# Optimization experiments

Measured on AMD Instinct MI355X. Metric: run time of the kernel, lower is better.

The kernel has to match this reference:

```python
import jax, jax.numpy as jnp
import numpy as np

PAD_IDX = 0
NEG_INF = -1e30

N_USERS, N_ITEMS, N_SUBJECTS, EMB_DIM = 100000, 100000, 10000, 16
B, L = 16384, 50


def setup_inputs() -> dict:
    key = jax.random.key(0)
    ks = jax.random.split(key, 10)
    subj_emb = jax.random.normal(ks[0], (N_SUBJECTS, EMB_DIM), dtype=jnp.float32) * 0.1
    subj_emb = subj_emb.at[PAD_IDX].set(0.0)  # padding_idx row is zeros in torch
    attn_w = jax.random.normal(ks[1], (EMB_DIM,), dtype=jnp.float32) * 0.25
    attn_b = jnp.zeros((), dtype=jnp.float32)
    user_bias = jax.random.normal(ks[2], (N_USERS,), dtype=jnp.float32) * 0.05
    item_bias = jax.random.normal(ks[3], (N_ITEMS,), dtype=jnp.float32) * 0.05
    global_bias = jnp.zeros((), dtype=jnp.float32)
    user_idx = jax.random.randint(ks[4], (B,), 0, N_USERS)
    item_idx = jax.random.randint(ks[5], (B,), 0, N_ITEMS)
    fav_subjects = jax.random.randint(ks[6], (B, L), 0, N_SUBJECTS)
    book_subjects = jax.random.randint(ks[7], (B, L), 0, N_SUBJECTS)
    return {
        "subj_emb": subj_emb, "attn_w": attn_w, "attn_b": attn_b,
        "user_bias": user_bias, "item_bias": item_bias, "global_bias": global_bias,
        "user_idx": user_idx, "item_idx": item_idx,
        "fav_subjects": fav_subjects, "book_subjects": book_subjects,
    }


def attention_pool(indices, subj_emb, attn_w, attn_b):
    embs = subj_emb[indices]                      # [B, L, D] gather
    scores = embs @ attn_w + attn_b               # [B, L] tiny linear (D->1)
    mask = indices != PAD_IDX                     # [B, L]
    has_real = jnp.any(mask, axis=1)              # [B]
    # rows with no real subjects get position 0 unmasked (torch per-row loop)
    safe_mask = mask.at[:, 0].set(mask[:, 0] | ~has_real)
    scores = jnp.where(safe_mask, scores, NEG_INF)
    weights = jax.nn.softmax(scores, axis=1)      # [B, L]
    pooled = jnp.einsum("bld,bl->bd", embs, weights)
    return pooled  # dropout is identity in eval mode


def reference(subj_emb, attn_w, attn_b, user_bias, item_bias, global_bias,
              user_idx, item_idx, fav_subjects, book_subjects):
    u_emb = attention_pool(fav_subjects, subj_emb, attn_w, attn_b)   # [B, D]
    i_emb = attention_pool(book_subjects, subj_emb, attn_w, attn_b)  # [B, D]
    dot = jnp.sum(u_emb * i_emb, axis=1)                             # [B]
    return dot + user_bias[user_idx] + item_bias[item_idx] + global_bias
```

## Files before the change

### kernel.cpp

```cpp
#include <hip/hip_runtime.h>
#include <math.h>


#define PAD_IDX 0
constexpr int D = 16;
constexpr int ROWS_PER_BLOCK = 32;
constexpr int THREADS = 256;
constexpr int L_MAX = 64;

__global__ __launch_bounds__(256) void exp_table_kernel(
    const float* __restrict__ subj_emb,
    const float* __restrict__ attn_w,
    const float* __restrict__ attn_b,
    float* __restrict__ exptab,
    int n_subj)
{
    const int s = blockIdx.x * blockDim.x + threadIdx.x;
    if (s >= n_subj) return;
    const float4* e = (const float4*)(subj_emb + (long)s * D);
    const float4* w = (const float4*)attn_w;
    float4 e0 = e[0], e1 = e[1], e2 = e[2], e3 = e[3];
    float4 w0 = w[0], w1 = w[1], w2 = w[2], w3 = w[3];
    float acc = e0.x * w0.x + e0.y * w0.y + e0.z * w0.z + e0.w * w0.w
              + e1.x * w1.x + e1.y * w1.y + e1.z * w1.z + e1.w * w1.w
              + e2.x * w2.x + e2.y * w2.y + e2.z * w2.z + e2.w * w2.w
              + e3.x * w3.x + e3.y * w3.y + e3.z * w3.z + e3.w * w3.w;
    exptab[s] = __expf(acc + attn_b[0]);
}

__global__ __launch_bounds__(256) void pool_kernel(
    const float* __restrict__ subj_emb,
    const float* __restrict__ exptab,
    const float* __restrict__ user_bias,
    const float* __restrict__ item_bias,
    const float* __restrict__ global_bias,
    const int*  __restrict__ user_idx,
    const int*  __restrict__ item_idx,
    const int*  __restrict__ fav_subjects,
    const int*  __restrict__ book_subjects,
    float* __restrict__ out,
    int B, int L)
{
    __shared__ int sidx[2][ROWS_PER_BLOCK * L_MAX];

    const int row0  = blockIdx.x * ROWS_PER_BLOCK;
    const int nInts = ROWS_PER_BLOCK * L;
    const long base = (long)row0 * L;

    {
        const int n4 = nInts >> 2;
        const int4* fsrc = (const int4*)(fav_subjects  + base);
        const int4* bsrc = (const int4*)(book_subjects + base);
        int4* fdst = (int4*)sidx[0];
        int4* bdst = (int4*)sidx[1];
        for (int i = threadIdx.x; i < n4; i += THREADS) {
            fdst[i] = fsrc[i];
            bdst[i] = bsrc[i];
        }
        for (int i = (n4 << 2) + threadIdx.x; i < nInts; i += THREADS) {
            sidx[0][i] = fav_subjects[base + i];
            sidx[1][i] = book_subjects[base + i];
        }
    }
    __syncthreads();

    const int t    = threadIdx.x;
    const int r    = t >> 3;
    const int pool = (t >> 2) & 1;
    const int j    = t & 3;
    const int row  = row0 + r;
    const bool valid = (row < B);

    const int* __restrict__ idxl = sidx[pool] + r * L;

    float4 acc = {0.f, 0.f, 0.f, 0.f};
    float  s   = 0.f;

    #pragma unroll 10
    for (int l = 0; l < L; ++l) {
        const int si = idxl[l];
        const float ew = exptab[si];
        const float4 e = *(const float4*)(subj_emb + (long)si * D + 4 * j);
        const float w = (si != PAD_IDX) ? ew : 0.f;
        s     += w;
        acc.x += w * e.x;
        acc.y += w * e.y;
        acc.z += w * e.z;
        acc.w += w * e.w;
    }

    const float inv = (s > 0.f) ? (1.f / s) : 0.f;
    float4 u;
    u.x = acc.x * inv; u.y = acc.y * inv; u.z = acc.z * inv; u.w = acc.w * inv;

    float4 o;
    o.x = __shfl_xor(u.x, 4, 8);
    o.y = __shfl_xor(u.y, 4, 8);
    o.z = __shfl_xor(u.z, 4, 8);
    o.w = __shfl_xor(u.w, 4, 8);

    float prod = u.x * o.x + u.y * o.y + u.z * o.z + u.w * o.w;
    prod += __shfl_xor(prod, 1, 4);
    prod += __shfl_xor(prod, 2, 4);

    if (valid && (t & 7) == 0) {
        out[row] = prod + user_bias[user_idx[row]]
                        + item_bias[item_idx[row]]
                        + global_bias[0];
    }
}

extern "C" void kernel_launch(void* const* d_in, const int* in_sizes, int n_in,
                              void* d_out, int out_size, void* d_ws, size_t ws_size,
                              hipStream_t stream) {
    const float* subj_emb    = (const float*)d_in[0];
    const float* attn_w      = (const float*)d_in[1];
    const float* attn_b      = (const float*)d_in[2];
    const float* user_bias   = (const float*)d_in[3];
    const float* item_bias   = (const float*)d_in[4];
    const float* global_bias = (const float*)d_in[5];
    const int*   user_idx    = (const int*)d_in[6];
    const int*   item_idx    = (const int*)d_in[7];
    const int*   fav_subj    = (const int*)d_in[8];
    const int*   book_subj   = (const int*)d_in[9];
    float*       out         = (float*)d_out;
    float*       exptab      = (float*)d_ws;

    const int n_subj = in_sizes[0] / D;
    const int B      = in_sizes[6];
    const int L      = in_sizes[8] / B;

    {
        const int blocks = (n_subj + 255) / 256;
        exp_table_kernel<<<blocks, 256, 0, stream>>>(
            subj_emb, attn_w, attn_b, exptab, n_subj);
    }
    {
        const int blocks = (B + ROWS_PER_BLOCK - 1) / ROWS_PER_BLOCK;
        pool_kernel<<<blocks, THREADS, 0, stream>>>(
            subj_emb, exptab, user_bias, item_bias, global_bias,
            user_idx, item_idx, fav_subj, book_subj, out, B, L);
    }
}
```

Measured before the change: 91.29 us.

## Split each row's subject loop across four thread groups with L specialization

Each pooled row is now handled by 32 threads instead of 8. Four groups of threads take interleaved subject positions and combine their partial sums with cross-lane shuffles, and blocks cover 8 rows instead of 32. A template specialization for L=50 fully unrolls the shortened loop, and a generic fallback kernel covers other lengths. The aim is more independent gathers in flight per row and a shorter serial dependency chain, at the cost of extra shuffle reductions and four times as many blocks.

```diff
diff --git a/kernel.cpp b/kernel.cpp
--- a/kernel.cpp
+++ b/kernel.cpp
@@ -4,9 +4,8 @@
 
 #define PAD_IDX 0
 constexpr int D = 16;
-constexpr int ROWS_PER_BLOCK = 32;
+constexpr int ROWS_PER_BLOCK = 8;
 constexpr int THREADS = 256;
-constexpr int L_MAX = 64;
 
 __global__ __launch_bounds__(256) void exp_table_kernel(
     const float* __restrict__ subj_emb,
@@ -28,6 +27,7 @@
     exptab[s] = __expf(acc + attn_b[0]);
 }
 
+template <int LFIX>
 __global__ __launch_bounds__(256) void pool_kernel(
     const float* __restrict__ subj_emb,
     const float* __restrict__ exptab,
@@ -39,13 +39,13 @@
     const int*  __restrict__ fav_subjects,
     const int*  __restrict__ book_subjects,
     float* __restrict__ out,
-    int B, int L)
+    int B)
 {
-    __shared__ int sidx[2][ROWS_PER_BLOCK * L_MAX];
+    __shared__ int sidx[2][ROWS_PER_BLOCK * LFIX];
 
     const int row0  = blockIdx.x * ROWS_PER_BLOCK;
-    const int nInts = ROWS_PER_BLOCK * L;
-    const long base = (long)row0 * L;
+    const int nInts = ROWS_PER_BLOCK * LFIX;
+    const long base = (long)row0 * LFIX;
 
     {
         const int n4 = nInts >> 2;
@@ -65,20 +65,22 @@
     __syncthreads();
 
     const int t    = threadIdx.x;
-    const int r    = t >> 3;
+    const int r    = t >> 5;
+    const int c    = (t >> 3) & 3;
     const int pool = (t >> 2) & 1;
     const int j    = t & 3;
     const int row  = row0 + r;
-    const bool valid = (row < B);
-
-    const int* __restrict__ idxl = sidx[pool] + r * L;
+
+    const int* __restrict__ idxl = sidx[pool] + r * LFIX;
 
     float4 acc = {0.f, 0.f, 0.f, 0.f};
     float  s   = 0.f;
 
-    #pragma unroll 10
-    for (int l = 0; l < L; ++l) {
-        const int si = idxl[l];
+    constexpr int ITERS = (LFIX + 3) / 4;
+    #pragma unroll
+    for (int k = 0; k < ITERS; ++k) {
+        const int l  = c + 4 * k;
+        const int si = (l < LFIX) ? idxl[l] : PAD_IDX;
         const float ew = exptab[si];
         const float4 e = *(const float4*)(subj_emb + (long)si * D + 4 * j);
         const float w = (si != PAD_IDX) ? ew : 0.f;
@@ -89,6 +91,12 @@
         acc.w += w * e.w;
     }
 
+    acc.x += __shfl_xor(acc.x, 8, 32);  acc.x += __shfl_xor(acc.x, 16, 32);
+    acc.y += __shfl_xor(acc.y, 8, 32);  acc.y += __shfl_xor(acc.y, 16, 32);
+    acc.z += __shfl_xor(acc.z, 8, 32);  acc.z += __shfl_xor(acc.z, 16, 32);
+    acc.w += __shfl_xor(acc.w, 8, 32);  acc.w += __shfl_xor(acc.w, 16, 32);
+    s     += __shfl_xor(s,     8, 32);  s     += __shfl_xor(s,     16, 32);
+
     const float inv = (s > 0.f) ? (1.f / s) : 0.f;
     float4 u;
     u.x = acc.x * inv; u.y = acc.y * inv; u.z = acc.z * inv; u.w = acc.w * inv;
@@ -103,10 +111,70 @@
     prod += __shfl_xor(prod, 1, 4);
     prod += __shfl_xor(prod, 2, 4);
 
-    if (valid && (t & 7) == 0) {
+    if (row < B && (t & 31) == 0) {
         out[row] = prod + user_bias[user_idx[row]]
                         + item_bias[item_idx[row]]
                         + global_bias[0];
+    }
+}
+
+__global__ __launch_bounds__(256) void pool_kernel_gen(
+    const float* __restrict__ subj_emb,
+    const float* __restrict__ exptab,
+    const float* __restrict__ user_bias,
+    const float* __restrict__ item_bias,
+    const float* __restrict__ global_bias,
+    const int*  __restrict__ user_idx,
+    const int*  __restrict__ item_idx,
+    const int*  __restrict__ fav_subjects,
+    const int*  __restrict__ book_subjects,
+    float* __restrict__ out,
+    int B, int L)
+{
+    __shared__ int sidx[2][ROWS_PER_BLOCK * 128];
+    const int row0  = blockIdx.x * ROWS_PER_BLOCK;
+    const int nInts = ROWS_PER_BLOCK * L;
+    const long base = (long)row0 * L;
+    for (int i = threadIdx.x; i < nInts; i += THREADS) {
+        sidx[0][i] = fav_subjects[base + i];
+        sidx[1][i] = book_subjects[base + i];
+    }
+    __syncthreads();
+
+    const int t    = threadIdx.x;
+    const int r    = t >> 5;
+    const int c    = (t >> 3) & 3;
+    const int pool = (t >> 2) & 1;
+    const int j    = t & 3;
+    const int row  = row0 + r;
+    const int* __restrict__ idxl = sidx[pool] + r * L;
+
+    float4 acc = {0.f, 0.f, 0.f, 0.f};
+    float  s   = 0.f;
+    for (int l = c; l < L; l += 4) {
+        const int si = idxl[l];
+        const float ew = exptab[si];
+        const float4 e = *(const float4*)(subj_emb + (long)si * D + 4 * j);
+        const float w = (si != PAD_IDX) ? ew : 0.f;
+        s += w;
+        acc.x += w * e.x; acc.y += w * e.y; acc.z += w * e.z; acc.w += w * e.w;
+    }
+    acc.x += __shfl_xor(acc.x, 8, 32);  acc.x += __shfl_xor(acc.x, 16, 32);
+    acc.y += __shfl_xor(acc.y, 8, 32);  acc.y += __shfl_xor(acc.y, 16, 32);
+    acc.z += __shfl_xor(acc.z, 8, 32);  acc.z += __shfl_xor(acc.z, 16, 32);
+    acc.w += __shfl_xor(acc.w, 8, 32);  acc.w += __shfl_xor(acc.w, 16, 32);
+    s     += __shfl_xor(s,     8, 32);  s     += __shfl_xor(s,     16, 32);
+    const float inv = (s > 0.f) ? (1.f / s) : 0.f;
+    float4 u = {acc.x * inv, acc.y * inv, acc.z * inv, acc.w * inv};
+    float4 o;
+    o.x = __shfl_xor(u.x, 4, 8); o.y = __shfl_xor(u.y, 4, 8);
+    o.z = __shfl_xor(u.z, 4, 8); o.w = __shfl_xor(u.w, 4, 8);
+    float prod = u.x * o.x + u.y * o.y + u.z * o.z + u.w * o.w;
+    prod += __shfl_xor(prod, 1, 4);
+    prod += __shfl_xor(prod, 2, 4);
+    if (row < B && (t & 31) == 0) {
+        out[row] = prod + user_bias[user_idx[row]]
+                        + item_bias[item_idx[row]] + global_bias[0];
     }
 }
 
@@ -135,9 +203,13 @@
         exp_table_kernel<<<blocks, 256, 0, stream>>>(
             subj_emb, attn_w, attn_b, exptab, n_subj);
     }
-    {
-        const int blocks = (B + ROWS_PER_BLOCK - 1) / ROWS_PER_BLOCK;
-        pool_kernel<<<blocks, THREADS, 0, stream>>>(
+    const int blocks = (B + ROWS_PER_BLOCK - 1) / ROWS_PER_BLOCK;
+    if (L == 50) {
+        pool_kernel<50><<<blocks, THREADS, 0, stream>>>(
+            subj_emb, exptab, user_bias, item_bias, global_bias,
+            user_idx, item_idx, fav_subj, book_subj, out, B);
+    } else {
+        pool_kernel_gen<<<blocks, THREADS, 0, stream>>>(
             subj_emb, exptab, user_bias, item_bias, global_bias,
             user_idx, item_idx, fav_subj, book_subj, out, B, L);
     }
```

Result: no change. 89.63 us (-1.8%).
